# Kernel optimization log

Hardware: AMD Instinct MI355X
Metric: run time of the kernel (lower is better)

The kernel has to match this reference:

```python
import jax, jax.numpy as jnp
import numpy as np

B_, S_, H_, O_ = 4, 2048, 2048, 2048
E_, R_ = 8, 16
LORA_ALPHA = 16.0


def setup_inputs() -> dict:
    key = jax.random.key(0)
    ks = jax.random.split(key, 5)
    x = jax.random.normal(ks[0], (B_, S_, H_), dtype=jnp.float32)
    W = jax.random.normal(ks[1], (O_, H_), dtype=jnp.float32) * 0.02   # frozen base weight [out, in]
    gate_w = jax.random.normal(ks[2], (E_, H_), dtype=jnp.float32) * 0.02  # router Linear weight [E, H]
    A = jax.random.normal(ks[3], (E_, R_, H_), dtype=jnp.float32) * 0.02   # stacked lora_A weights [E, r, in]
    B = jax.random.normal(ks[4], (E_, O_, R_), dtype=jnp.float32) * 0.02   # stacked lora_B weights [E, out, r]
    return {"x": x, "W": W, "gate_w": gate_w, "A": A, "B": B}


def reference(x, W, gate_w, A, B):
    bsz, seq, hid = x.shape
    E = gate_w.shape[0]
    x_flat = x.reshape(-1, hid)                                  # [T, H]

    # base linear
    out = x_flat @ W.T                                           # [T, O]

    # learned router: softmax -> top-2 -> renormalize
    logits = x_flat @ gate_w.T                                   # [T, E]
    probs = jax.nn.softmax(logits, axis=-1)
    topk_w, topk_idx = jax.lax.top_k(probs, 2)                   # [T, 2]
    topk_w = topk_w / jnp.sum(topk_w, axis=-1, keepdims=True)

    # per-token per-expert combine weight (sum over the 2 slots), scaled by alpha
    onehot = jax.nn.one_hot(topk_idx, E, dtype=x.dtype)          # [T, 2, E]
    wmat = jnp.einsum('tk,tke->te', topk_w, onehot) * LORA_ALPHA # [T, E]

    # dense grouped LoRA: h_e = x A_e^T ; out += sum_e w_te * (h_e B_e^T)
    h = jnp.einsum('th,erh->etr', x_flat, A)                     # [E, T, r]
    hw = h * wmat.T[:, :, None]                                  # [E, T, r]
    lora = jnp.einsum('etr,eor->to', hw, B)                      # [T, O]

    return (out + lora).reshape(bsz, seq, -1)
```

## Files before the change

kernel.cpp:

```cpp
#include <hip/hip_runtime.h>
#include <hip/hip_bf16.h>
#include <stdint.h>

#define T_TOK 8192
#define HID   2048
#define OUTD  2048
#define NE    8
#define RR    16
#define KAUG  2176
#define NH    128

typedef __bf16 bf16x8 __attribute__((ext_vector_type(8)));
typedef float  f32x4  __attribute__((ext_vector_type(4)));

#define AS1(p) ((__attribute__((address_space(1))) void*)(p))
#define AS3(p) ((__attribute__((address_space(3))) void*)(p))

__device__ inline unsigned short f2bf(float f) {
  unsigned int u = __builtin_bit_cast(unsigned int, f);
  unsigned int r = (u + 0x7fffu + ((u >> 16) & 1u)) >> 16;
  return (unsigned short)r;
}

__device__ inline ushort4 f2bf4(float4 v) {
  ushort4 u;
  u.x = f2bf(v.x); u.y = f2bf(v.y); u.z = f2bf(v.z); u.w = f2bf(v.w);
  return u;
}

__global__ __launch_bounds__(256) void k_xrl(const float* __restrict__ x,
                                             const float* __restrict__ gw,
                                             unsigned short* __restrict__ Xa,
                                             float* __restrict__ wte) {
  int w = threadIdx.x >> 6, lane = threadIdx.x & 63;
  int t = blockIdx.x * 4 + w;
  const float* xt = x + (size_t)t * HID;
  unsigned short* xo = Xa + (size_t)t * KAUG;
  double acc[8] = {0, 0, 0, 0, 0, 0, 0, 0};
#pragma unroll
  for (int i = 0; i < 8; ++i) {
    int k = (i * 64 + lane) * 4;
    float4 xv = *(const float4*)(xt + k);
    *(ushort4*)(xo + k) = f2bf4(xv);
#pragma unroll
    for (int e = 0; e < 8; ++e) {
      float4 gv = *(const float4*)(gw + (size_t)e * HID + k);
      acc[e] += (double)xv.x * gv.x + (double)xv.y * gv.y +
                (double)xv.z * gv.z + (double)xv.w * gv.w;
    }
  }
#pragma unroll
  for (int off = 32; off >= 1; off >>= 1)
#pragma unroll
    for (int e = 0; e < 8; ++e)
      acc[e] += __shfl_down(acc[e], off, 64);
  if (lane == 0) {
    int e0 = 0; double l0 = acc[0];
#pragma unroll
    for (int e = 1; e < 8; ++e) if (acc[e] > l0) { l0 = acc[e]; e0 = e; }
    int e1 = -1; double l1 = -1e300;
#pragma unroll
    for (int e = 0; e < 8; ++e) if (e != e0 && acc[e] > l1) { l1 = acc[e]; e1 = e; }
    double w0 = 16.0 / (1.0 + exp(l1 - l0));
    float o[8] = {0.f, 0.f, 0.f, 0.f, 0.f, 0.f, 0.f, 0.f};
    o[e0] = (float)w0;
    o[e1] = (float)(16.0 - w0);
    float4* p = (float4*)(wte + (size_t)t * 8);
    p[0] = make_float4(o[0], o[1], o[2], o[3]);
    p[1] = make_float4(o[4], o[5], o[6], o[7]);
  }
}

__global__ void k_wba(const float* __restrict__ W, const float* __restrict__ Bw,
                      const float* __restrict__ A,
                      unsigned short* __restrict__ Wa, unsigned short* __restrict__ Ag) {
  int b = blockIdx.x;
  if (b < 4096) {
    int tid = b * 256 + threadIdx.x;
    int row = tid >> 9, c = (tid & 511) << 2;
    float4 v = *(const float4*)(W + (size_t)row * HID + c);
    *(ushort4*)(Wa + (size_t)row * KAUG + c) = f2bf4(v);
  } else if (b < 4352) {
    int tid = (b - 4096) * 256 + threadIdx.x;
    int o = tid >> 5, j = (tid & 31) << 2;
    int e = j >> 4, r = j & 15;
    float4 v = *(const float4*)(Bw + (size_t)e * OUTD * RR + (size_t)o * RR + r);
    *(ushort4*)(Wa + (size_t)o * KAUG + 2048 + j) = f2bf4(v);
  } else {
    int tid = (b - 4352) * 256 + threadIdx.x;
    float4 v = *(const float4*)(A + (size_t)tid * 4);
    *(ushort4*)(Ag + (size_t)tid * 4) = f2bf4(v);
  }
}

__global__ __launch_bounds__(256) void k_ha(const unsigned short* __restrict__ Xa,
                                            const unsigned short* __restrict__ Ag,
                                            const float* __restrict__ wte,
                                            unsigned short* __restrict__ XaW) {
  __shared__ unsigned short Xs[32 * 64];
  __shared__ unsigned short As[64 * 64];
  int tm = (blockIdx.x >> 1) * 32;
  int ch = (blockIdx.x & 1) * 64;
  int w = threadIdx.x >> 6, lane = threadIdx.x & 63;
  int lrow = lane >> 3;
  int lcol_s = (lane & 7) << 3;
  int lcol_g = ((lane & 7) ^ (lrow & 7)) << 3;

  const unsigned short* gX = Xa + (size_t)(tm + w * 8 + lrow) * KAUG + lcol_g;
  const unsigned short* gA = Ag + (size_t)(ch + w * 16 + lrow) * HID + lcol_g;
  unsigned short* sX = Xs + (w * 8 + lrow) * 64 + lcol_s;
  unsigned short* sA = As + (w * 16 + lrow) * 64 + lcol_s;

  f32x4 acc[2] = {};
  for (int kt = 0; kt < HID; kt += 64) {
    __builtin_amdgcn_global_load_lds(AS1(gX), AS3(sX), 16, 0, 0);
#pragma unroll
    for (int i = 0; i < 2; ++i)
      __builtin_amdgcn_global_load_lds(AS1(gA + (size_t)i * 8 * HID), AS3(sA + i * 8 * 64), 16, 0, 0);
    __syncthreads();
#pragma unroll
    for (int ks = 0; ks < 2; ++ks) {
      int kch = ks * 4 + (lane >> 4);
      int ko = ((kch ^ (lane & 7)) << 3);
      bf16x8 a = *(const bf16x8*)(Xs + ((w >> 1) * 16 + (lane & 15)) * 64 + ko);
#pragma unroll
      for (int fn = 0; fn < 2; ++fn) {
        bf16x8 bv = *(const bf16x8*)(As + ((w & 1) * 32 + fn * 16 + (lane & 15)) * 64 + ko);
        acc[fn] = __builtin_amdgcn_mfma_f32_16x16x32_bf16(a, bv, acc[fn], 0, 0, 0);
      }
    }
    __syncthreads();
    gX += 64; gA += 64;
  }
  int q = lane >> 4;
#pragma unroll
  for (int fn = 0; fn < 2; ++fn) {
    int col = ch + (w & 1) * 32 + fn * 16 + (lane & 15);
    int e = col >> 4;
#pragma unroll
    for (int r = 0; r < 4; ++r) {
      int t = tm + (w >> 1) * 16 + q * 4 + r;
      float we = wte[(size_t)t * 8 + e];
      XaW[(size_t)t * KAUG + 2048 + col] = f2bf(we * acc[fn][r]);
    }
  }
}

__global__ __launch_bounds__(256, 4) void k_gemm(const unsigned short* __restrict__ Xa,
                                                 const unsigned short* __restrict__ Wa,
                                                 float* __restrict__ out) {
  __shared__ unsigned short As[128 * 64];
  __shared__ unsigned short Bs[128 * 64];
  int lid = blockIdx.x;
  int xcd = lid & 7, s = lid >> 3;
  int bm = (xcd * 8 + (s & 7)) * 128;
  int bn = (s >> 3) * 128;
  int w = threadIdx.x >> 6, lane = threadIdx.x & 63;
  int wm = (w >> 1) * 64, wn = (w & 1) * 64;
  int lrow = lane >> 3;
  int lcol_s = (lane & 7) << 3;
  int lcol_g = ((lane & 7) ^ (lrow & 7)) << 3;

  const unsigned short* gA = Xa + (size_t)(bm + w * 32 + lrow) * KAUG + lcol_g;
  const unsigned short* gB = Wa + (size_t)(bn + w * 32 + lrow) * KAUG + lcol_g;
  unsigned short* sA = As + (w * 32 + lrow) * 64 + lcol_s;
  unsigned short* sB = Bs + (w * 32 + lrow) * 64 + lcol_s;

  f32x4 acc[4][4] = {};
  for (int kt = 0; kt < KAUG; kt += 64) {
#pragma unroll
    for (int i = 0; i < 4; ++i) {
      __builtin_amdgcn_global_load_lds(AS1(gA + (size_t)i * 8 * KAUG), AS3(sA + i * 8 * 64), 16, 0, 0);
      __builtin_amdgcn_global_load_lds(AS1(gB + (size_t)i * 8 * KAUG), AS3(sB + i * 8 * 64), 16, 0, 0);
    }
    __syncthreads();
#pragma unroll
    for (int ks = 0; ks < 2; ++ks) {
      int kch = ks * 4 + (lane >> 4);
      int ko = ((kch ^ (lane & 7)) << 3);
      bf16x8 a[4], b[4];
#pragma unroll
      for (int f = 0; f < 4; ++f) a[f] = *(const bf16x8*)(As + (wm + f * 16 + (lane & 15)) * 64 + ko);
#pragma unroll
      for (int f = 0; f < 4; ++f) b[f] = *(const bf16x8*)(Bs + (wn + f * 16 + (lane & 15)) * 64 + ko);
#pragma unroll
      for (int fm = 0; fm < 4; ++fm)
#pragma unroll
        for (int fn = 0; fn < 4; ++fn)
          acc[fm][fn] = __builtin_amdgcn_mfma_f32_16x16x32_bf16(a[fm], b[fn], acc[fm][fn], 0, 0, 0);
    }
    __syncthreads();
    gA += 64; gB += 64;
  }
#pragma unroll
  for (int fm = 0; fm < 4; ++fm) {
    int row = bm + wm + fm * 16 + ((lane >> 4) << 2);
#pragma unroll
    for (int r = 0; r < 4; ++r) {
      float* orow = out + (size_t)(row + r) * OUTD + bn + wn + (lane & 15);
#pragma unroll
      for (int fn = 0; fn < 4; ++fn) orow[fn * 16] = acc[fm][fn][r];
    }
  }
}

extern "C" void kernel_launch(void* const* d_in, const int* in_sizes, int n_in,
                              void* d_out, int out_size, void* d_ws, size_t ws_size,
                              hipStream_t stream) {
  const float* x  = (const float*)d_in[0];
  const float* W  = (const float*)d_in[1];
  const float* gw = (const float*)d_in[2];
  const float* A  = (const float*)d_in[3];
  const float* B  = (const float*)d_in[4];
  float* out = (float*)d_out;

  char* ws = (char*)d_ws;
  unsigned short* Xa  = (unsigned short*)(ws);
  unsigned short* Wa  = (unsigned short*)(ws + 35651584);
  unsigned short* Ag  = (unsigned short*)(ws + 44564480);
  float*          wte = (float*)        (ws + 45088768);

  k_xrl <<<2048, 256, 0, stream>>>(x, gw, Xa, wte);
  k_wba <<<4608, 256, 0, stream>>>(W, B, A, Wa, Ag);
  k_ha  <<<512, 256, 0, stream>>>(Xa, Ag, wte, Xa);
  k_gemm<<<1024, 256, 0, stream>>>(Xa, Wa, out);
}
```

Baseline: 246.1 us.

## Merge prep kernels, stage router weights in LDS, multi-buffer k_ha loads

Fuses the router/x-conversion kernel and the weight-conversion kernel into one launch. The router blocks now stage gate weights in shared memory and handle 8 tokens per 512-thread block, instead of re-reading them from global memory. The k_ha LoRA-A kernel gets a 4-slot LDS ring with three loads in flight, using explicit vmcnt waits and raw barriers instead of a single-buffered load/sync loop. This trades one launch and some latency for 64KB of LDS in the prep blocks (which limits occupancy) and fragile hand-counted waitcnt logic.

```diff
diff --git a/kernel.cpp b/kernel.cpp
--- a/kernel.cpp
+++ b/kernel.cpp
@@ -28,68 +28,78 @@
   return u;
 }
 
-__global__ __launch_bounds__(256) void k_xrl(const float* __restrict__ x,
-                                             const float* __restrict__ gw,
-                                             unsigned short* __restrict__ Xa,
-                                             float* __restrict__ wte) {
-  int w = threadIdx.x >> 6, lane = threadIdx.x & 63;
-  int t = blockIdx.x * 4 + w;
-  const float* xt = x + (size_t)t * HID;
-  unsigned short* xo = Xa + (size_t)t * KAUG;
-  double acc[8] = {0, 0, 0, 0, 0, 0, 0, 0};
-#pragma unroll
-  for (int i = 0; i < 8; ++i) {
-    int k = (i * 64 + lane) * 4;
-    float4 xv = *(const float4*)(xt + k);
-    *(ushort4*)(xo + k) = f2bf4(xv);
-#pragma unroll
-    for (int e = 0; e < 8; ++e) {
-      float4 gv = *(const float4*)(gw + (size_t)e * HID + k);
-      acc[e] += (double)xv.x * gv.x + (double)xv.y * gv.y +
-                (double)xv.z * gv.z + (double)xv.w * gv.w;
-    }
-  }
-#pragma unroll
-  for (int off = 32; off >= 1; off >>= 1)
-#pragma unroll
-    for (int e = 0; e < 8; ++e)
-      acc[e] += __shfl_down(acc[e], off, 64);
-  if (lane == 0) {
-    int e0 = 0; double l0 = acc[0];
-#pragma unroll
-    for (int e = 1; e < 8; ++e) if (acc[e] > l0) { l0 = acc[e]; e0 = e; }
-    int e1 = -1; double l1 = -1e300;
-#pragma unroll
-    for (int e = 0; e < 8; ++e) if (e != e0 && acc[e] > l1) { l1 = acc[e]; e1 = e; }
-    double w0 = 16.0 / (1.0 + exp(l1 - l0));
-    float o[8] = {0.f, 0.f, 0.f, 0.f, 0.f, 0.f, 0.f, 0.f};
-    o[e0] = (float)w0;
-    o[e1] = (float)(16.0 - w0);
-    float4* p = (float4*)(wte + (size_t)t * 8);
-    p[0] = make_float4(o[0], o[1], o[2], o[3]);
-    p[1] = make_float4(o[4], o[5], o[6], o[7]);
-  }
-}
-
-__global__ void k_wba(const float* __restrict__ W, const float* __restrict__ Bw,
-                      const float* __restrict__ A,
-                      unsigned short* __restrict__ Wa, unsigned short* __restrict__ Ag) {
-  int b = blockIdx.x;
-  if (b < 4096) {
-    int tid = b * 256 + threadIdx.x;
-    int row = tid >> 9, c = (tid & 511) << 2;
-    float4 v = *(const float4*)(W + (size_t)row * HID + c);
-    *(ushort4*)(Wa + (size_t)row * KAUG + c) = f2bf4(v);
-  } else if (b < 4352) {
-    int tid = (b - 4096) * 256 + threadIdx.x;
-    int o = tid >> 5, j = (tid & 31) << 2;
-    int e = j >> 4, r = j & 15;
-    float4 v = *(const float4*)(Bw + (size_t)e * OUTD * RR + (size_t)o * RR + r);
-    *(ushort4*)(Wa + (size_t)o * KAUG + 2048 + j) = f2bf4(v);
+__global__ __launch_bounds__(512) void k_prep(const float* __restrict__ x,
+                                              const float* __restrict__ gw,
+                                              const float* __restrict__ W,
+                                              const float* __restrict__ Bw,
+                                              const float* __restrict__ A,
+                                              unsigned short* __restrict__ Xa,
+                                              float* __restrict__ wte,
+                                              unsigned short* __restrict__ Wa,
+                                              unsigned short* __restrict__ Ag) {
+  __shared__ float gws[NE * HID];
+  if (blockIdx.x < 1024) {
+#pragma unroll
+    for (int i = 0; i < 8; ++i) {
+      int idx = (i * 512 + (int)threadIdx.x) * 4;
+      *(float4*)(gws + idx) = *(const float4*)(gw + idx);
+    }
+    __syncthreads();
+    int w = threadIdx.x >> 6, lane = threadIdx.x & 63;
+    int t = blockIdx.x * 8 + w;
+    const float* xt = x + (size_t)t * HID;
+    unsigned short* xo = Xa + (size_t)t * KAUG;
+    double acc[8] = {0, 0, 0, 0, 0, 0, 0, 0};
+#pragma unroll
+    for (int i = 0; i < 8; ++i) {
+      int k = (i * 64 + lane) * 4;
+      float4 xv = *(const float4*)(xt + k);
+      *(ushort4*)(xo + k) = f2bf4(xv);
+#pragma unroll
+      for (int e = 0; e < 8; ++e) {
+        float4 gv = *(const float4*)(gws + e * HID + k);
+        acc[e] += (double)xv.x * gv.x + (double)xv.y * gv.y +
+                  (double)xv.z * gv.z + (double)xv.w * gv.w;
+      }
+    }
+#pragma unroll
+    for (int off = 32; off >= 1; off >>= 1)
+#pragma unroll
+      for (int e = 0; e < 8; ++e)
+        acc[e] += __shfl_down(acc[e], off, 64);
+    if (lane == 0) {
+      int e0 = 0; double l0 = acc[0];
+#pragma unroll
+      for (int e = 1; e < 8; ++e) if (acc[e] > l0) { l0 = acc[e]; e0 = e; }
+      int e1 = -1; double l1 = -1e300;
+#pragma unroll
+      for (int e = 0; e < 8; ++e) if (e != e0 && acc[e] > l1) { l1 = acc[e]; e1 = e; }
+      double w0 = 16.0 / (1.0 + exp(l1 - l0));
+      float o[8] = {0.f, 0.f, 0.f, 0.f, 0.f, 0.f, 0.f, 0.f};
+      o[e0] = (float)w0;
+      o[e1] = (float)(16.0 - w0);
+      float4* p = (float4*)(wte + (size_t)t * 8);
+      p[0] = make_float4(o[0], o[1], o[2], o[3]);
+      p[1] = make_float4(o[4], o[5], o[6], o[7]);
+    }
   } else {
-    int tid = (b - 4352) * 256 + threadIdx.x;
-    float4 v = *(const float4*)(A + (size_t)tid * 4);
-    *(ushort4*)(Ag + (size_t)tid * 4) = f2bf4(v);
+    int b2 = blockIdx.x - 1024;
+    if (b2 < 2048) {
+      int tid = b2 * 512 + threadIdx.x;
+      int row = tid >> 9, c = (tid & 511) << 2;
+      float4 v = *(const float4*)(W + (size_t)row * HID + c);
+      *(ushort4*)(Wa + (size_t)row * KAUG + c) = f2bf4(v);
+    } else if (b2 < 2176) {
+      int tid = (b2 - 2048) * 512 + threadIdx.x;
+      int o = tid >> 5, j = (tid & 31) << 2;
+      int e = j >> 4, r = j & 15;
+      float4 v = *(const float4*)(Bw + (size_t)e * OUTD * RR + (size_t)o * RR + r);
+      *(ushort4*)(Wa + (size_t)o * KAUG + 2048 + j) = f2bf4(v);
+    } else {
+      int tid = (b2 - 2176) * 512 + threadIdx.x;
+      float4 v = *(const float4*)(A + (size_t)tid * 4);
+      *(ushort4*)(Ag + (size_t)tid * 4) = f2bf4(v);
+    }
   }
 }
 
@@ -97,8 +107,8 @@
                                             const unsigned short* __restrict__ Ag,
                                             const float* __restrict__ wte,
                                             unsigned short* __restrict__ XaW) {
-  __shared__ unsigned short Xs[32 * 64];
-  __shared__ unsigned short As[64 * 64];
+  __shared__ unsigned short Xs[4][32 * 64];
+  __shared__ unsigned short As[4][64 * 64];
   int tm = (blockIdx.x >> 1) * 32;
   int ch = (blockIdx.x & 1) * 64;
   int w = threadIdx.x >> 6, lane = threadIdx.x & 63;
@@ -108,30 +118,54 @@
 
   const unsigned short* gX = Xa + (size_t)(tm + w * 8 + lrow) * KAUG + lcol_g;
   const unsigned short* gA = Ag + (size_t)(ch + w * 16 + lrow) * HID + lcol_g;
-  unsigned short* sX = Xs + (w * 8 + lrow) * 64 + lcol_s;
-  unsigned short* sA = As + (w * 16 + lrow) * 64 + lcol_s;
+  int sxo = (w * 8 + lrow) * 64 + lcol_s;
+  int sao = (w * 16 + lrow) * 64 + lcol_s;
 
   f32x4 acc[2] = {};
-  for (int kt = 0; kt < HID; kt += 64) {
-    __builtin_amdgcn_global_load_lds(AS1(gX), AS3(sX), 16, 0, 0);
-#pragma unroll
-    for (int i = 0; i < 2; ++i)
-      __builtin_amdgcn_global_load_lds(AS1(gA + (size_t)i * 8 * HID), AS3(sA + i * 8 * 64), 16, 0, 0);
-    __syncthreads();
-#pragma unroll
-    for (int ks = 0; ks < 2; ++ks) {
-      int kch = ks * 4 + (lane >> 4);
-      int ko = ((kch ^ (lane & 7)) << 3);
-      bf16x8 a = *(const bf16x8*)(Xs + ((w >> 1) * 16 + (lane & 15)) * 64 + ko);
-#pragma unroll
-      for (int fn = 0; fn < 2; ++fn) {
-        bf16x8 bv = *(const bf16x8*)(As + ((w & 1) * 32 + fn * 16 + (lane & 15)) * 64 + ko);
-        acc[fn] = __builtin_amdgcn_mfma_f32_16x16x32_bf16(a, bv, acc[fn], 0, 0, 0);
-      }
-    }
-    __syncthreads();
-    gX += 64; gA += 64;
-  }
+
+#define HA_STAGE(slot, koff) do {                                                         \
+    __builtin_amdgcn_global_load_lds(AS1(gX + (koff)), AS3(&Xs[slot][0] + sxo), 16, 0, 0);\
+    __builtin_amdgcn_global_load_lds(AS1(gA + (koff)), AS3(&As[slot][0] + sao), 16, 0, 0);\
+    __builtin_amdgcn_global_load_lds(AS1(gA + (size_t)8 * HID + (koff)),                  \
+                                     AS3(&As[slot][0] + 8 * 64 + sao), 16, 0, 0);         \
+  } while (0)
+
+#define HA_COMP(s) do {                                                                   \
+    _Pragma("unroll")                                                                     \
+    for (int ks = 0; ks < 2; ++ks) {                                                      \
+      int kch = ks * 4 + (lane >> 4);                                                     \
+      int ko = ((kch ^ (lane & 7)) << 3);                       \
+      bf16x8 a = *(const bf16x8*)(&Xs[s][0] + ((w >> 1) * 16 + (lane & 15)) * 64 + ko);   \
+      _Pragma("unroll")                                                                   \
+      for (int fn = 0; fn < 2; ++fn) {                                                    \
+        bf16x8 bv = *(const bf16x8*)(&As[s][0] + ((w & 1) * 32 + fn * 16 + (lane & 15)) * 64 + ko); \
+        acc[fn] = __builtin_amdgcn_mfma_f32_16x16x32_bf16(a, bv, acc[fn], 0, 0, 0);       \
+      }                                                                                   \
+    }                                                                                     \
+  } while (0)
+
+  HA_STAGE(0, 0);
+  HA_STAGE(1, 64);
+  HA_STAGE(2, 128);
+  for (int t = 0; t < 29; ++t) {
+    asm volatile("s_waitcnt vmcnt(6)" ::: "memory");
+    __builtin_amdgcn_s_barrier();
+    HA_COMP(t & 3);
+    __builtin_amdgcn_s_barrier();
+    HA_STAGE((t + 3) & 3, (t + 3) * 64);
+  }
+  asm volatile("s_waitcnt vmcnt(6)" ::: "memory");
+  __builtin_amdgcn_s_barrier();
+  HA_COMP(1);
+  asm volatile("s_waitcnt vmcnt(3)" ::: "memory");
+  __builtin_amdgcn_s_barrier();
+  HA_COMP(2);
+  asm volatile("s_waitcnt vmcnt(0)" ::: "memory");
+  __builtin_amdgcn_s_barrier();
+  HA_COMP(3);
+#undef HA_STAGE
+#undef HA_COMP
+
   int q = lane >> 4;
 #pragma unroll
   for (int fn = 0; fn < 2; ++fn) {
@@ -220,8 +254,7 @@
   unsigned short* Ag  = (unsigned short*)(ws + 44564480);
   float*          wte = (float*)        (ws + 45088768);
 
-  k_xrl <<<2048, 256, 0, stream>>>(x, gw, Xa, wte);
-  k_wba <<<4608, 256, 0, stream>>>(W, B, A, Wa, Ag);
+  k_prep<<<3328, 512, 0, stream>>>(x, gw, W, B, A, Xa, wte, Wa, Ag);
   k_ha  <<<512, 256, 0, stream>>>(Xa, Ag, wte, Xa);
   k_gemm<<<1024, 256, 0, stream>>>(Xa, Wa, out);
 }
```

Result: faster. 220.7 us (-10.3%).
